# Performance work log

Measured on AMD Instinct MI355X. Metric: run time of the kernel, lower is better.

The kernel has to match this reference:

```python
import jax, jax.numpy as jnp
import numpy as np
from jax import lax

EMBED = 200
HID = 300
NCLASS = 2
B = 64
S = 255          # complete binary tree: 2**8 - 1 nodes
DEPTH = 8        # levels 0..7, root at node 0
VOCAB = 32000


def make_tree():
    parent = np.zeros(S, np.int32)
    parent[0] = S  # sentinel: root has no parent (dropped via dummy segment)
    for i in range(1, S):
        parent[i] = (i - 1) // 2
    depth = np.floor(np.log2(np.arange(S) + 1)).astype(np.int32)
    return jnp.asarray(parent), jnp.asarray(depth)


def setup_inputs() -> dict:
    key = jax.random.key(0)
    ks = jax.random.split(key, 8)
    parent, depth = make_tree()
    return {
        "x": jax.random.randint(ks[0], (S, B), 0, VOCAB, dtype=jnp.int32),
        "parent": parent,
        "depth": depth,
        "embed": jax.random.normal(ks[1], (VOCAB, EMBED), jnp.float32) * 0.1,
        "W_iou": jax.random.normal(ks[2], (EMBED, 3 * HID), jnp.float32) * 0.05,
        "U_iou": jax.random.normal(ks[3], (HID, 3 * HID), jnp.float32) * 0.05,
        "b_iou": jnp.zeros((3 * HID,), jnp.float32),
        "W_f": jax.random.normal(ks[4], (EMBED, HID), jnp.float32) * 0.05,
        "U_f": jax.random.normal(ks[5], (HID, HID), jnp.float32) * 0.05,
        "b_f": jnp.zeros((HID,), jnp.float32),
        "W_out": jax.random.normal(ks[6], (HID, NCLASS), jnp.float32) * 0.05,
        "b_out": jnp.zeros((NCLASS,), jnp.float32),
    }


def reference(x, parent, depth, embed, W_iou, U_iou, b_iou, W_f, U_f, b_f, W_out, b_out):
    # x: [S, B] token ids (seq-major, as in the torch model)
    emb = embed[x]                              # [S, B, E]
    wx_iou = emb @ W_iou + b_iou                # [S, B, 3H] input contributions
    wx_f = emb @ W_f + b_f                      # [S, B, H]
    seg = jnp.minimum(parent, S)                # root -> dummy segment S
    pidx = jnp.clip(parent, 0, S - 1)           # safe gather index for parent's x-part

    H0 = jnp.zeros((S, B, HID), emb.dtype)
    C0 = jnp.zeros((S, B, HID), emb.dtype)

    def level_step(carry, d):
        H, C = carry
        child = (depth == d + 1)[:, None, None].astype(H.dtype)   # nodes feeding level d
        # child-sum of hidden states into parents
        h_sum = jax.ops.segment_sum(H * child, seg, num_segments=S + 1)[:S]  # [S,B,H]
        # per-child forget gate: sigma(W_f x_parent + U_f h_child + b_f)
        f = jax.nn.sigmoid(wx_f[pidx] + H @ U_f)                  # [S,B,H]
        fc = jax.ops.segment_sum(f * C * child, seg, num_segments=S + 1)[:S]
        iou = wx_iou + h_sum @ U_iou                              # [S,B,3H]
        i_g, o_g, u_g = jnp.split(iou, 3, axis=-1)
        i_g = jax.nn.sigmoid(i_g)
        o_g = jax.nn.sigmoid(o_g)
        u_g = jnp.tanh(u_g)
        c_new = i_g * u_g + fc
        h_new = o_g * jnp.tanh(c_new)
        node = (depth == d)[:, None, None]
        H = jnp.where(node, h_new, H)
        C = jnp.where(node, c_new, C)
        return (H, C), None

    levels = jnp.arange(DEPTH - 1, -1, -1)      # process deepest level first
    (H, C), _ = lax.scan(level_step, (H0, C0), levels)

    tree_hidden = H[0]                          # [B, H] root hidden state
    logits = tree_hidden @ W_out + b_out        # Linear(hidden_dim, n_class)
    return jax.nn.log_softmax(logits, axis=-1)  # [B, 2]
```

## Files before the change

kernel.cpp:

```cpp
#include <hip/hip_runtime.h>
#include <hip/hip_bf16.h>
#include <math.h>

#define NS 255
#define NB 64
#define NE 200
#define NH 300
#define TS 2048
#define HTS 1024


typedef __attribute__((ext_vector_type(8))) short short8;
typedef __attribute__((ext_vector_type(4))) float f32x4;

__device__ __forceinline__ float sigmoidf_(float x) { return 1.0f / (1.0f + __expf(-x)); }
__device__ __forceinline__ unsigned short f2bf(float v) {
    union { __hip_bfloat16 b; unsigned short u; } cv; cv.b = __float2bfloat16(v); return cv.u;
}
__device__ __forceinline__ float bf2f(unsigned short u) {
    union { unsigned short u; __hip_bfloat16 b; } cv; cv.u = u; return __bfloat162float(cv.b);
}
__device__ __forceinline__ unsigned short f2h(float v) {
    union { _Float16 h; unsigned short u; } cv; cv.h = (_Float16)v; return cv.u;
}
__device__ __forceinline__ float h2f(unsigned short u) {
    union { unsigned short u; _Float16 h; } cv; cv.u = u; return (float)cv.h;
}
__device__ __forceinline__ int swz(int row, int kk) {
    int g = (kk >> 3) ^ ((row >> 1) & 3);
    return ((row << 2) + g) * 8 + (kk & 7);
}

__global__ __launch_bounds__(256) void prep_kernel(
    const float* __restrict__ U_iou, const float* __restrict__ U_f,
    const float* __restrict__ W_iou, const float* __restrict__ W_f,
    const float* __restrict__ embed, const int* __restrict__ x,
    unsigned short* __restrict__ BW, unsigned short* __restrict__ AembT)
{
    const int gBW = 4 * 5 * 17 * 256;
    const int gAe = NS * 7 * 256;
    int total = gBW + gAe;
    int stride = gridDim.x * blockDim.x;
    for (int gi = blockIdx.x * blockDim.x + threadIdx.x; gi < total; gi += stride) {
        unsigned short st[8];
        if (gi < gBW) {
            int gg = gi & 255, tile = gi >> 8;
            int row = gg >> 2, pos = gg & 3;
            int kk0 = (pos ^ ((row >> 1) & 3)) << 3;
            int c = tile % 17, t2 = tile / 17;
            int s = t2 % 5, g4 = t2 / 5;
            int j = s * 64 + row;
#pragma unroll
            for (int u = 0; u < 8; ++u) {
                int kk = kk0 + u; float v = 0.f;
                if (c < 7) {
                    int k = c * 32 + kk;
                    if (j < NH && k < NE)
                        v = (g4 < 3) ? W_iou[k * 900 + g4 * NH + j] : W_f[k * NH + j];
                } else {
                    int k = (c - 7) * 32 + kk;
                    if (j < NH && k < NH)
                        v = (g4 < 3) ? U_iou[k * 900 + g4 * NH + j] : U_f[k * NH + j];
                }
                st[u] = f2bf(v);
            }
            *(short8*)(BW + (size_t)tile * TS + (row * 4 + pos) * 8) = *(short8*)st;
        } else {
            int gi2 = gi - gBW;
            int gg = gi2 & 255, tile = gi2 >> 8;
            int row = gg >> 2, pos = gg & 3;
            int kk0 = (pos ^ ((row >> 1) & 3)) << 3;
            int c = tile % 7, node = tile / 7;
            int k0 = c * 32 + kk0;
            const float* er = embed + (size_t)x[node * NB + row] * NE;
#pragma unroll
            for (int u = 0; u < 8; ++u)
                st[u] = (k0 + u < NE) ? f2bf(er[k0 + u]) : (unsigned short)0;
            *(short8*)(AembT + (size_t)tile * TS + (row * 4 + pos) * 8) = *(short8*)st;
        }
    }
}

template<int NCH, int SA>
__device__ __forceinline__ void gemm2(f32x4 acc[4][2],
    const unsigned short* __restrict__ A, const unsigned short* __restrict__ B)
{
#pragma unroll
    for (int c = 0; c < NCH; ++c) {
        const unsigned short* At = A + c * SA;
        const unsigned short* Bt = B + c * TS;
        short8 a0 = *(const short8*)(At);
        short8 a1 = *(const short8*)(At + 512);
#pragma unroll
        for (int t = 0; t < 4; ++t) {
            short8 b = *(const short8*)(Bt + t * 512);
            acc[t][0] = __builtin_amdgcn_mfma_f32_16x16x32_bf16(a0, b, acc[t][0], 0, 0, 0);
            acc[t][1] = __builtin_amdgcn_mfma_f32_16x16x32_bf16(a1, b, acc[t][1], 0, 0, 0);
        }
    }
}
template<int NCH>
__device__ __forceinline__ void gemm_f(f32x4 acc[4][4],
    const unsigned short* __restrict__ A, const unsigned short* __restrict__ B)
{
#pragma unroll
    for (int c = 0; c < NCH; ++c) {
        const unsigned short* At = A + c * TS;
        const unsigned short* Bt = B + c * TS;
        short8 a0 = *(const short8*)(At);
        short8 a1 = *(const short8*)(At + 512);
        short8 a2 = *(const short8*)(At + 1024);
        short8 a3 = *(const short8*)(At + 1536);
#pragma unroll
        for (int t = 0; t < 4; ++t) {
            short8 b = *(const short8*)(Bt + t * 512);
            acc[t][0] = __builtin_amdgcn_mfma_f32_16x16x32_bf16(a0, b, acc[t][0], 0, 0, 0);
            acc[t][1] = __builtin_amdgcn_mfma_f32_16x16x32_bf16(a1, b, acc[t][1], 0, 0, 0);
            acc[t][2] = __builtin_amdgcn_mfma_f32_16x16x32_bf16(a2, b, acc[t][2], 0, 0, 0);
            acc[t][3] = __builtin_amdgcn_mfma_f32_16x16x32_bf16(a3, b, acc[t][3], 0, 0, 0);
        }
    }
}

__global__ __launch_bounds__(320) void level_kernel(
    const unsigned short* __restrict__ AembT, const unsigned short* __restrict__ BW,
    const float* __restrict__ b_iou, const float* __restrict__ b_f,
    unsigned short* __restrict__ HbfT, unsigned short* __restrict__ Cg,
    int base, int m, int sh)
{
    __shared__ unsigned short sm[24 * HTS];
    int bid = blockIdx.x;
    int p, s, half;
    if (m > 0) {
        int xcd = bid & 7, idx = bid >> 3;
        int o = idx % m, rest = idx / m;
        p = base + xcd * m + o;
        s = rest % 5; half = rest / 5;
    } else {
        int xcd = bid & 7;
        if (xcd & ((1 << sh) - 1)) return;
        p = base + (xcd >> sh);
        int idx = bid >> 3;
        s = idx % 5; half = idx / 5;
    }
    int tid = threadIdx.x;
    int w = tid >> 6, lane = tid & 63, ln = lane & 15, quad = lane >> 4;
    int l = 2 * p + 1, r = 2 * p + 2;
    int bsel = (w < 4) ? w : 3;
    int gq = (quad ^ ((ln >> 1) & 3)) * 8;
    int offA = (half * 32 + ln) * 32 + gq;
    int offL = ln * 32 + gq;
    int offB = ln * 32 + gq;

    for (int idx = w; idx < 24; idx += 5) {
        const unsigned short* gsrc;
        if (idx < 20) {
            int node = (idx < 10) ? l : r;
            int tt = (idx < 10) ? idx : idx - 10;
            gsrc = HbfT + ((size_t)node * 10 + tt) * TS + half * HTS;
        } else {
            int ii = idx - 20;
            int node = (ii < 2) ? l : r;
            gsrc = Cg + ((size_t)node * 10 + 2 * s + (ii & 1)) * TS + half * HTS;
        }
        unsigned short* ldst = sm + idx * HTS;
#pragma unroll
        for (int u = 0; u < 2; ++u)
            __builtin_amdgcn_global_load_lds(
                (const __attribute__((address_space(1))) unsigned short*)(gsrc + u * 512 + lane * 8),
                (__attribute__((address_space(3))) unsigned short*)(ldst + u * 512 + lane * 8),
                16, 0, 0);
    }

    f32x4 acc[4][2];
#pragma unroll
    for (int t = 0; t < 4; ++t)
#pragma unroll
        for (int q = 0; q < 2; ++q) acc[t][q] = (f32x4){0.f, 0.f, 0.f, 0.f};

    const unsigned short* Bsrc = BW + (size_t)(bsel * 5 + s) * 17 * TS;
    const unsigned short* Ae = AembT + (size_t)p * 7 * TS;
    gemm2<7, TS>(acc, Ae + offA, Bsrc + offB);

    __syncthreads();

    const unsigned short* BH = Bsrc + 7 * TS + offB;
    if (w < 3) {
        gemm2<10, HTS>(acc, sm + offL, BH);
        gemm2<10, HTS>(acc, sm + 10 * HTS + offL, BH);
    } else if (w == 3) {
        gemm2<10, HTS>(acc, sm + offL, BH);
    } else {
        gemm2<10, HTS>(acc, sm + 10 * HTS + offL, BH);
    }

    float* smf = (float*)sm;
    for (int t = 0; t < 4; ++t) {
        __syncthreads();
#pragma unroll
        for (int ms = 0; ms < 2; ++ms)
#pragma unroll
            for (int rr = 0; rr < 4; ++rr)
                smf[w * 544 + (ms * 16 + quad * 4 + rr) * 17 + ln] = acc[t][ms][rr];
        __syncthreads();
        for (int idx2 = tid; idx2 < 512; idx2 += 320) {
            int mm = idx2 >> 4, n = idx2 & 15;
            int gm = half * 32 + mm;
            int jj = s * 64 + t * 16 + n;
            bool ok = jj < NH;
            float pi = smf[0 * 544 + mm * 17 + n] + (ok ? b_iou[jj] : 0.f);
            float po = smf[1 * 544 + mm * 17 + n] + (ok ? b_iou[NH + jj] : 0.f);
            float pu = smf[2 * 544 + mm * 17 + n] + (ok ? b_iou[2 * NH + jj] : 0.f);
            float bj = ok ? b_f[jj] : 0.f;
            float fl = sigmoidf_(smf[3 * 544 + mm * 17 + n] + bj);
            float fr = sigmoidf_(smf[4 * 544 + mm * 17 + n] + bj);
            int xr = (mm >> 1) & 3;
            int cel = (mm * 4 + ((((t & 1) * 2) + (n >> 3)) ^ xr)) * 8 + (n & 7);
            int ts2 = t >> 1;
            float cl = h2f(sm[(20 + ts2) * HTS + cel]);
            float cr = h2f(sm[(22 + ts2) * HTS + cel]);
            float cc = sigmoidf_(pi) * tanhf(pu) + fl * cl + fr * cr;
            float hh = sigmoidf_(po) * tanhf(cc);
            size_t tbase = ((size_t)p * 10 + (jj >> 5)) * TS + swz(gm, jj & 31);
            if (ok) Cg[tbase] = f2h(cc);
            HbfT[tbase] = ok ? f2bf(hh) : (unsigned short)0;
        }
    }
}

__global__ __launch_bounds__(192) void leaf_kernel(
    const unsigned short* __restrict__ AembT, const unsigned short* __restrict__ BW,
    const float* __restrict__ b_iou,
    unsigned short* __restrict__ HbfT, unsigned short* __restrict__ Cg, int m)
{
    int bid = blockIdx.x;
    int xcd = bid & 7, idx = bid >> 3;
    int o = idx % m, rest = idx / m;
    int p = 127 + xcd * m + o;
    int s = rest % 5;
    int tid = threadIdx.x;
    int w = tid >> 6, lane = tid & 63, ln = lane & 15, quad = lane >> 4;
    int off = ln * 32 + (quad ^ ((ln >> 1) & 3)) * 8;

    const unsigned short* Bsrc = BW + (size_t)(w * 5 + s) * 17 * TS;
    const unsigned short* Ae = AembT + (size_t)p * 7 * TS;

    f32x4 acc[4][4];
#pragma unroll
    for (int t = 0; t < 4; ++t)
#pragma unroll
        for (int q = 0; q < 4; ++q) acc[t][q] = (f32x4){0.f, 0.f, 0.f, 0.f};

    gemm_f<7>(acc, Ae + off, Bsrc + off);

    __shared__ float tile[3][64][16];
    for (int t = 0; t < 4; ++t) {
        __syncthreads();
#pragma unroll
        for (int ms = 0; ms < 4; ++ms)
#pragma unroll
            for (int rr = 0; rr < 4; ++rr)
                tile[w][ms * 16 + quad * 4 + rr][ln] = acc[t][ms][rr];
        __syncthreads();
        for (int idx2 = tid; idx2 < 1024; idx2 += 192) {
            int mm = idx2 >> 4, n = idx2 & 15;
            int jj = s * 64 + t * 16 + n;
            bool ok = jj < NH;
            float pi = tile[0][mm][n] + (ok ? b_iou[jj] : 0.f);
            float po = tile[1][mm][n] + (ok ? b_iou[NH + jj] : 0.f);
            float pu = tile[2][mm][n] + (ok ? b_iou[2 * NH + jj] : 0.f);
            float cc = sigmoidf_(pi) * tanhf(pu);
            float hh = sigmoidf_(po) * tanhf(cc);
            size_t tbase = ((size_t)p * 10 + (jj >> 5)) * TS + swz(mm, jj & 31);
            if (ok) Cg[tbase] = f2h(cc);
            HbfT[tbase] = ok ? f2bf(hh) : (unsigned short)0;
        }
    }
}

__global__ __launch_bounds__(64) void out_kernel(
    const unsigned short* __restrict__ HbfT,
    const float* __restrict__ W_out, const float* __restrict__ b_out,
    float* __restrict__ out)
{
    int b = threadIdx.x;
    float l0 = 0.f, l1 = 0.f;
#pragma unroll 4
    for (int k = 0; k < NH; ++k) {
        float hk = bf2f(HbfT[(size_t)(k >> 5) * TS + swz(b, k & 31)]);
        l0 += hk * W_out[k * 2];
        l1 += hk * W_out[k * 2 + 1];
    }
    l0 += b_out[0];
    l1 += b_out[1];
    float m = fmaxf(l0, l1);
    float lse = m + logf(__expf(l0 - m) + __expf(l1 - m));
    out[b * 2 + 0] = l0 - lse;
    out[b * 2 + 1] = l1 - lse;
}

extern "C" void kernel_launch(void* const* d_in, const int* in_sizes, int n_in,
                              void* d_out, int out_size, void* d_ws, size_t ws_size,
                              hipStream_t stream)
{
    const int*   x     = (const int*)d_in[0];
    const float* embed = (const float*)d_in[3];
    const float* W_iou = (const float*)d_in[4];
    const float* U_iou = (const float*)d_in[5];
    const float* b_iou = (const float*)d_in[6];
    const float* W_f   = (const float*)d_in[7];
    const float* U_f   = (const float*)d_in[8];
    const float* b_f   = (const float*)d_in[9];
    const float* W_out = (const float*)d_in[10];
    const float* b_out = (const float*)d_in[11];

    char* ws = (char*)d_ws;
    unsigned short* HbfT  = (unsigned short*)(ws + 0);
    unsigned short* Cg    = (unsigned short*)(ws + 10444800);
    unsigned short* AembT = (unsigned short*)(ws + 20889600);
    unsigned short* BW    = (unsigned short*)(ws + 28200960);

    prep_kernel<<<4096, 256, 0, stream>>>(U_iou, U_f, W_iou, W_f, embed, x, BW, AembT);

    leaf_kernel<<<640, 192, 0, stream>>>(AembT, BW, b_iou, HbfT, Cg, 16);
    for (int d = 6; d >= 3; --d) {
        int base = (1 << d) - 1;
        int m = 1 << (d - 3);
        level_kernel<<<80 * m, 320, 0, stream>>>(AembT, BW, b_iou, b_f, HbfT, Cg,
                                                 base, m, 0);
    }
    for (int d = 2; d >= 0; --d) {
        level_kernel<<<80, 320, 0, stream>>>(AembT, BW, b_iou, b_f, HbfT, Cg,
                                             (1 << d) - 1, 0, 3 - d);
    }
    out_kernel<<<1, 64, 0, stream>>>(HbfT, W_out, b_out, (float*)d_out);
}
```

Before: 274.9 us.

## Fuse all tree-LSTM stages into one persistent kernel with grid barriers

Merges the prep, leaf, seven per-level and output kernels into a single persistent kernel of 512 blocks. Stages are separated by a custom two-phase atomic grid barrier in which eight leader blocks gather arrivals, so the inter-launch gaps are removed. In exchange the level work is mapped onto a fixed grid, leaf work now runs with 320 threads where only three waves compute, and correctness depends on all 512 blocks being co-resident and on the barrier's memory ordering.

```diff
diff --git a/kernel.cpp b/kernel.cpp
--- a/kernel.cpp
+++ b/kernel.cpp
@@ -8,6 +8,7 @@
 #define NH 300
 #define TS 2048
 #define HTS 1024
+#define NBLK 512
 
 
 typedef __attribute__((ext_vector_type(8))) short short8;
@@ -31,54 +32,20 @@
     return ((row << 2) + g) * 8 + (kk & 7);
 }
 
-__global__ __launch_bounds__(256) void prep_kernel(
-    const float* __restrict__ U_iou, const float* __restrict__ U_f,
-    const float* __restrict__ W_iou, const float* __restrict__ W_f,
-    const float* __restrict__ embed, const int* __restrict__ x,
-    unsigned short* __restrict__ BW, unsigned short* __restrict__ AembT)
-{
-    const int gBW = 4 * 5 * 17 * 256;
-    const int gAe = NS * 7 * 256;
-    int total = gBW + gAe;
-    int stride = gridDim.x * blockDim.x;
-    for (int gi = blockIdx.x * blockDim.x + threadIdx.x; gi < total; gi += stride) {
-        unsigned short st[8];
-        if (gi < gBW) {
-            int gg = gi & 255, tile = gi >> 8;
-            int row = gg >> 2, pos = gg & 3;
-            int kk0 = (pos ^ ((row >> 1) & 3)) << 3;
-            int c = tile % 17, t2 = tile / 17;
-            int s = t2 % 5, g4 = t2 / 5;
-            int j = s * 64 + row;
-#pragma unroll
-            for (int u = 0; u < 8; ++u) {
-                int kk = kk0 + u; float v = 0.f;
-                if (c < 7) {
-                    int k = c * 32 + kk;
-                    if (j < NH && k < NE)
-                        v = (g4 < 3) ? W_iou[k * 900 + g4 * NH + j] : W_f[k * NH + j];
-                } else {
-                    int k = (c - 7) * 32 + kk;
-                    if (j < NH && k < NH)
-                        v = (g4 < 3) ? U_iou[k * 900 + g4 * NH + j] : U_f[k * NH + j];
-                }
-                st[u] = f2bf(v);
-            }
-            *(short8*)(BW + (size_t)tile * TS + (row * 4 + pos) * 8) = *(short8*)st;
-        } else {
-            int gi2 = gi - gBW;
-            int gg = gi2 & 255, tile = gi2 >> 8;
-            int row = gg >> 2, pos = gg & 3;
-            int kk0 = (pos ^ ((row >> 1) & 3)) << 3;
-            int c = tile % 7, node = tile / 7;
-            int k0 = c * 32 + kk0;
-            const float* er = embed + (size_t)x[node * NB + row] * NE;
-#pragma unroll
-            for (int u = 0; u < 8; ++u)
-                st[u] = (k0 + u < NE) ? f2bf(er[k0 + u]) : (unsigned short)0;
-            *(short8*)(AembT + (size_t)tile * TS + (row * 4 + pos) * 8) = *(short8*)st;
-        }
-    }
+__device__ __forceinline__ void gbar(int* c1, int* c2, int tid, int bid) {
+    __syncthreads();
+    if (tid == 0) {
+        __hip_atomic_fetch_add(c1, 1, __ATOMIC_RELAXED, __HIP_MEMORY_SCOPE_AGENT);
+        if (bid < 8) {
+            while (__hip_atomic_load(c1, __ATOMIC_RELAXED, __HIP_MEMORY_SCOPE_AGENT) < NBLK)
+                __builtin_amdgcn_s_sleep(2);
+            __builtin_amdgcn_fence(__ATOMIC_RELEASE, "agent");
+            __hip_atomic_fetch_add(c2, 1, __ATOMIC_RELAXED, __HIP_MEMORY_SCOPE_AGENT);
+        }
+        while (__hip_atomic_load(c2, __ATOMIC_RELAXED, __HIP_MEMORY_SCOPE_AGENT) < 8)
+            __builtin_amdgcn_s_sleep(2);
+    }
+    __syncthreads();
 }
 
 template<int NCH, int SA>
@@ -122,28 +89,13 @@
     }
 }
 
-__global__ __launch_bounds__(320) void level_kernel(
+__device__ __forceinline__ void do_internal(unsigned short* sm,
+    int p, int s, int half, int tid,
     const unsigned short* __restrict__ AembT, const unsigned short* __restrict__ BW,
     const float* __restrict__ b_iou, const float* __restrict__ b_f,
-    unsigned short* __restrict__ HbfT, unsigned short* __restrict__ Cg,
-    int base, int m, int sh)
-{
-    __shared__ unsigned short sm[24 * HTS];
-    int bid = blockIdx.x;
-    int p, s, half;
-    if (m > 0) {
-        int xcd = bid & 7, idx = bid >> 3;
-        int o = idx % m, rest = idx / m;
-        p = base + xcd * m + o;
-        s = rest % 5; half = rest / 5;
-    } else {
-        int xcd = bid & 7;
-        if (xcd & ((1 << sh) - 1)) return;
-        p = base + (xcd >> sh);
-        int idx = bid >> 3;
-        s = idx % 5; half = idx / 5;
-    }
-    int tid = threadIdx.x;
+    unsigned short* __restrict__ HbfT, unsigned short* __restrict__ Cg)
+{
+    __syncthreads();
     int w = tid >> 6, lane = tid & 63, ln = lane & 15, quad = lane >> 4;
     int l = 2 * p + 1, r = 2 * p + 2;
     int bsel = (w < 4) ? w : 3;
@@ -228,47 +180,44 @@
     }
 }
 
-__global__ __launch_bounds__(192) void leaf_kernel(
-    const unsigned short* __restrict__ AembT, const unsigned short* __restrict__ BW,
-    const float* __restrict__ b_iou,
-    unsigned short* __restrict__ HbfT, unsigned short* __restrict__ Cg, int m)
-{
-    int bid = blockIdx.x;
-    int xcd = bid & 7, idx = bid >> 3;
-    int o = idx % m, rest = idx / m;
-    int p = 127 + xcd * m + o;
-    int s = rest % 5;
-    int tid = threadIdx.x;
+__device__ __forceinline__ void do_leaf(unsigned short* sm, int p, int s,
+    int tid, const unsigned short* __restrict__ AembT,
+    const unsigned short* __restrict__ BW, const float* __restrict__ b_iou,
+    unsigned short* __restrict__ HbfT, unsigned short* __restrict__ Cg)
+{
+    __syncthreads();
     int w = tid >> 6, lane = tid & 63, ln = lane & 15, quad = lane >> 4;
     int off = ln * 32 + (quad ^ ((ln >> 1) & 3)) * 8;
 
-    const unsigned short* Bsrc = BW + (size_t)(w * 5 + s) * 17 * TS;
-    const unsigned short* Ae = AembT + (size_t)p * 7 * TS;
-
     f32x4 acc[4][4];
 #pragma unroll
     for (int t = 0; t < 4; ++t)
 #pragma unroll
         for (int q = 0; q < 4; ++q) acc[t][q] = (f32x4){0.f, 0.f, 0.f, 0.f};
 
-    gemm_f<7>(acc, Ae + off, Bsrc + off);
-
-    __shared__ float tile[3][64][16];
+    if (w < 3) {
+        const unsigned short* Bsrc = BW + (size_t)(w * 5 + s) * 17 * TS;
+        const unsigned short* Ae = AembT + (size_t)p * 7 * TS;
+        gemm_f<7>(acc, Ae + off, Bsrc + off);
+    }
+
+    float* tile = (float*)sm;
     for (int t = 0; t < 4; ++t) {
         __syncthreads();
-#pragma unroll
-        for (int ms = 0; ms < 4; ++ms)
-#pragma unroll
-            for (int rr = 0; rr < 4; ++rr)
-                tile[w][ms * 16 + quad * 4 + rr][ln] = acc[t][ms][rr];
+        if (w < 3)
+#pragma unroll
+            for (int ms = 0; ms < 4; ++ms)
+#pragma unroll
+                for (int rr = 0; rr < 4; ++rr)
+                    tile[(w * 64 + ms * 16 + quad * 4 + rr) * 16 + ln] = acc[t][ms][rr];
         __syncthreads();
-        for (int idx2 = tid; idx2 < 1024; idx2 += 192) {
+        for (int idx2 = tid; idx2 < 1024; idx2 += 320) {
             int mm = idx2 >> 4, n = idx2 & 15;
             int jj = s * 64 + t * 16 + n;
             bool ok = jj < NH;
-            float pi = tile[0][mm][n] + (ok ? b_iou[jj] : 0.f);
-            float po = tile[1][mm][n] + (ok ? b_iou[NH + jj] : 0.f);
-            float pu = tile[2][mm][n] + (ok ? b_iou[2 * NH + jj] : 0.f);
+            float pi = tile[(0 * 64 + mm) * 16 + n] + (ok ? b_iou[jj] : 0.f);
+            float po = tile[(1 * 64 + mm) * 16 + n] + (ok ? b_iou[NH + jj] : 0.f);
+            float pu = tile[(2 * 64 + mm) * 16 + n] + (ok ? b_iou[2 * NH + jj] : 0.f);
             float cc = sigmoidf_(pi) * tanhf(pu);
             float hh = sigmoidf_(po) * tanhf(cc);
             size_t tbase = ((size_t)p * 10 + (jj >> 5)) * TS + swz(mm, jj & 31);
@@ -278,25 +227,108 @@
     }
 }
 
-__global__ __launch_bounds__(64) void out_kernel(
-    const unsigned short* __restrict__ HbfT,
+__global__ __launch_bounds__(320, 4) void fused_kernel(
+    const float* __restrict__ U_iou, const float* __restrict__ U_f,
+    const float* __restrict__ W_iou, const float* __restrict__ W_f,
+    const float* __restrict__ embed, const int* __restrict__ x,
+    const float* __restrict__ b_iou, const float* __restrict__ b_f,
     const float* __restrict__ W_out, const float* __restrict__ b_out,
-    float* __restrict__ out)
-{
-    int b = threadIdx.x;
-    float l0 = 0.f, l1 = 0.f;
+    unsigned short* __restrict__ BW, unsigned short* __restrict__ AembT,
+    unsigned short* __restrict__ HbfT, unsigned short* __restrict__ Cg,
+    float* __restrict__ out, int* __restrict__ bar)
+{
+    __shared__ unsigned short sm[24 * HTS];
+    int bid = blockIdx.x;
+    int tid = threadIdx.x;
+
+    {
+        const int gBW = 4 * 5 * 17 * 256;
+        const int gAe = NS * 7 * 256;
+        int total = gBW + gAe;
+        int stride = NBLK * 320;
+        for (int gi = bid * 320 + tid; gi < total; gi += stride) {
+            unsigned short st[8];
+            if (gi < gBW) {
+                int gg = gi & 255, tile = gi >> 8;
+                int row = gg >> 2, pos = gg & 3;
+                int kk0 = (pos ^ ((row >> 1) & 3)) << 3;
+                int c = tile % 17, t2 = tile / 17;
+                int s = t2 % 5, g4 = t2 / 5;
+                int j = s * 64 + row;
+#pragma unroll
+                for (int u = 0; u < 8; ++u) {
+                    int kk = kk0 + u; float v = 0.f;
+                    if (c < 7) {
+                        int k = c * 32 + kk;
+                        if (j < NH && k < NE)
+                            v = (g4 < 3) ? W_iou[k * 900 + g4 * NH + j] : W_f[k * NH + j];
+                    } else {
+                        int k = (c - 7) * 32 + kk;
+                        if (j < NH && k < NH)
+                            v = (g4 < 3) ? U_iou[k * 900 + g4 * NH + j] : U_f[k * NH + j];
+                    }
+                    st[u] = f2bf(v);
+                }
+                *(short8*)(BW + (size_t)tile * TS + (row * 4 + pos) * 8) = *(short8*)st;
+            } else {
+                int gi2 = gi - gBW;
+                int gg = gi2 & 255, tile = gi2 >> 8;
+                int row = gg >> 2, pos = gg & 3;
+                int kk0 = (pos ^ ((row >> 1) & 3)) << 3;
+                int c = tile % 7, node = tile / 7;
+                int k0 = c * 32 + kk0;
+                const float* er = embed + (size_t)x[node * NB + row] * NE;
+#pragma unroll
+                for (int u = 0; u < 8; ++u)
+                    st[u] = (k0 + u < NE) ? f2bf(er[k0 + u]) : (unsigned short)0;
+                *(short8*)(AembT + (size_t)tile * TS + (row * 4 + pos) * 8) = *(short8*)st;
+            }
+        }
+    }
+    gbar(bar + 0, bar + 1, tid, bid);
+
+    int xcd = bid & 7, slot = bid >> 3;
+
+    for (int t = slot; t < 80; t += 64)
+        do_leaf(sm, 127 + xcd * 16 + (t & 15), t >> 4, tid, AembT, BW, b_iou, HbfT, Cg);
+    gbar(bar + 2, bar + 3, tid, bid);
+
+    int bi = 4;
+    for (int d = 6; d >= 3; --d) {
+        int base = (1 << d) - 1;
+        int m = 1 << (d - 3);
+        int T = m * 10;
+        for (int t = slot; t < T; t += 64) {
+            int o = t % m, rest = t / m;
+            do_internal(sm, base + xcd * m + o, rest % 5, rest / 5,
+                        tid, AembT, BW, b_iou, b_f, HbfT, Cg);
+        }
+        gbar(bar + bi, bar + bi + 1, tid, bid); bi += 2;
+    }
+    for (int d = 2; d >= 0; --d) {
+        int n = 1 << d, sh = 3 - d;
+        if ((xcd & ((1 << sh) - 1)) == 0 && (xcd >> sh) < n && slot < 10)
+            do_internal(sm, n - 1 + (xcd >> sh), slot % 5, slot / 5,
+                        tid, AembT, BW, b_iou, b_f, HbfT, Cg);
+        gbar(bar + bi, bar + bi + 1, tid, bid); bi += 2;
+    }
+
+    if (bid == 0 && tid < NB) {
+        int b = tid;
+        float l0 = 0.f, l1 = 0.f;
 #pragma unroll 4
-    for (int k = 0; k < NH; ++k) {
-        float hk = bf2f(HbfT[(size_t)(k >> 5) * TS + swz(b, k & 31)]);
-        l0 += hk * W_out[k * 2];
-        l1 += hk * W_out[k * 2 + 1];
-    }
-    l0 += b_out[0];
-    l1 += b_out[1];
-    float m = fmaxf(l0, l1);
-    float lse = m + logf(__expf(l0 - m) + __expf(l1 - m));
-    out[b * 2 + 0] = l0 - lse;
-    out[b * 2 + 1] = l1 - lse;
+        for (int k = 0; k < NH; ++k) {
+            float hk = bf2f(HbfT[(size_t)(k >> 5) * TS + swz(b, k & 31)]);
+            l0 += hk * W_out[k * 2];
+            l1 += hk * W_out[k * 2 + 1];
+        }
+        l0 += b_out[0];
+        l1 += b_out[1];
+        float mx = fmaxf(l0, l1);
+        float lse = mx + logf(__expf(l0 - mx) + __expf(l1 - mx));
+        out[b * 2 + 0] = l0 - lse;
+        out[b * 2 + 1] = l1 - lse;
+    }
 }
 
 extern "C" void kernel_launch(void* const* d_in, const int* in_sizes, int n_in,
@@ -319,19 +351,11 @@
     unsigned short* Cg    = (unsigned short*)(ws + 10444800);
     unsigned short* AembT = (unsigned short*)(ws + 20889600);
     unsigned short* BW    = (unsigned short*)(ws + 28200960);
-
-    prep_kernel<<<4096, 256, 0, stream>>>(U_iou, U_f, W_iou, W_f, embed, x, BW, AembT);
-
-    leaf_kernel<<<640, 192, 0, stream>>>(AembT, BW, b_iou, HbfT, Cg, 16);
-    for (int d = 6; d >= 3; --d) {
-        int base = (1 << d) - 1;
-        int m = 1 << (d - 3);
-        level_kernel<<<80 * m, 320, 0, stream>>>(AembT, BW, b_iou, b_f, HbfT, Cg,
-                                                 base, m, 0);
-    }
-    for (int d = 2; d >= 0; --d) {
-        level_kernel<<<80, 320, 0, stream>>>(AembT, BW, b_iou, b_f, HbfT, Cg,
-                                             (1 << d) - 1, 0, 3 - d);
-    }
-    out_kernel<<<1, 64, 0, stream>>>(HbfT, W_out, b_out, (float*)d_out);
-}
+    int*            bar   = (int*)(ws + 29593600);
+
+    hipMemsetAsync(bar, 0, 128, stream);
+    fused_kernel<<<NBLK, 320, 0, stream>>>(U_iou, U_f, W_iou, W_f, embed, x,
+                                           b_iou, b_f, W_out, b_out,
+                                           BW, AembT, HbfT, Cg,
+                                           (float*)d_out, bar);
+}
```

After: 618.6 us. 2.25x slower.

## Fuse embedding gather into GEMMs and merge upper tree levels into persistent kernel

Applied to the files above, without the earlier changes.

Removes the precomputed bf16 embedding tile buffer: leaf and level kernels now gather embedding rows directly and convert to bf16 while loading MFMA operands. The five upper tree levels (depth 4 down to root) plus the output head are fused into one persistent 160-block kernel that uses global atomic counters as grid barriers, with agent-scope stores for H/C. This is meant to cut launch overhead and the prep pass that wrote the embedding tiles. In exchange it adds unswizzled scalar float gathers in the GEMM loop and relies on all 160 blocks being co-resident for the spin barriers.

```diff
diff --git a/kernel.cpp b/kernel.cpp
--- a/kernel.cpp
+++ b/kernel.cpp
@@ -30,67 +30,62 @@
     int g = (kk >> 3) ^ ((row >> 1) & 3);
     return ((row << 2) + g) * 8 + (kk & 7);
 }
+__device__ __forceinline__ void st_u16(unsigned short* p, unsigned short v) {
+    __hip_atomic_store(p, v, __ATOMIC_RELAXED, __HIP_MEMORY_SCOPE_AGENT);
+}
 
 __global__ __launch_bounds__(256) void prep_kernel(
     const float* __restrict__ U_iou, const float* __restrict__ U_f,
     const float* __restrict__ W_iou, const float* __restrict__ W_f,
-    const float* __restrict__ embed, const int* __restrict__ x,
-    unsigned short* __restrict__ BW, unsigned short* __restrict__ AembT)
-{
-    const int gBW = 4 * 5 * 17 * 256;
-    const int gAe = NS * 7 * 256;
-    int total = gBW + gAe;
-    int stride = gridDim.x * blockDim.x;
-    for (int gi = blockIdx.x * blockDim.x + threadIdx.x; gi < total; gi += stride) {
-        unsigned short st[8];
-        if (gi < gBW) {
-            int gg = gi & 255, tile = gi >> 8;
-            int row = gg >> 2, pos = gg & 3;
-            int kk0 = (pos ^ ((row >> 1) & 3)) << 3;
-            int c = tile % 17, t2 = tile / 17;
-            int s = t2 % 5, g4 = t2 / 5;
-            int j = s * 64 + row;
-#pragma unroll
-            for (int u = 0; u < 8; ++u) {
-                int kk = kk0 + u; float v = 0.f;
-                if (c < 7) {
-                    int k = c * 32 + kk;
-                    if (j < NH && k < NE)
-                        v = (g4 < 3) ? W_iou[k * 900 + g4 * NH + j] : W_f[k * NH + j];
-                } else {
-                    int k = (c - 7) * 32 + kk;
-                    if (j < NH && k < NH)
-                        v = (g4 < 3) ? U_iou[k * 900 + g4 * NH + j] : U_f[k * NH + j];
-                }
-                st[u] = f2bf(v);
-            }
-            *(short8*)(BW + (size_t)tile * TS + (row * 4 + pos) * 8) = *(short8*)st;
+    unsigned short* __restrict__ BW)
+{
+    int gi = blockIdx.x * blockDim.x + threadIdx.x;
+    if (gi >= 4 * 5 * 17 * 256) return;
+    unsigned short st[8];
+    int gg = gi & 255, tile = gi >> 8;
+    int row = gg >> 2, pos = gg & 3;
+    int kk0 = (pos ^ ((row >> 1) & 3)) << 3;
+    int c = tile % 17, t2 = tile / 17;
+    int s = t2 % 5, g4 = t2 / 5;
+    int j = s * 64 + row;
+#pragma unroll
+    for (int u = 0; u < 8; ++u) {
+        int kk = kk0 + u; float v = 0.f;
+        if (c < 7) {
+            int k = c * 32 + kk;
+            if (j < NH && k < NE)
+                v = (g4 < 3) ? W_iou[k * 900 + g4 * NH + j] : W_f[k * NH + j];
         } else {
-            int gi2 = gi - gBW;
-            int gg = gi2 & 255, tile = gi2 >> 8;
-            int row = gg >> 2, pos = gg & 3;
-            int kk0 = (pos ^ ((row >> 1) & 3)) << 3;
-            int c = tile % 7, node = tile / 7;
-            int k0 = c * 32 + kk0;
-            const float* er = embed + (size_t)x[node * NB + row] * NE;
-#pragma unroll
-            for (int u = 0; u < 8; ++u)
-                st[u] = (k0 + u < NE) ? f2bf(er[k0 + u]) : (unsigned short)0;
-            *(short8*)(AembT + (size_t)tile * TS + (row * 4 + pos) * 8) = *(short8*)st;
-        }
-    }
-}
-
-template<int NCH, int SA>
-__device__ __forceinline__ void gemm2(f32x4 acc[4][2],
-    const unsigned short* __restrict__ A, const unsigned short* __restrict__ B)
-{
-#pragma unroll
-    for (int c = 0; c < NCH; ++c) {
-        const unsigned short* At = A + c * SA;
+            int k = (c - 7) * 32 + kk;
+            if (j < NH && k < NH)
+                v = (g4 < 3) ? U_iou[k * 900 + g4 * NH + j] : U_f[k * NH + j];
+        }
+        st[u] = f2bf(v);
+    }
+    *(short8*)(BW + (size_t)tile * TS + (row * 4 + pos) * 8) = *(short8*)st;
+}
+
+__device__ __forceinline__ short8 ldcvt(const float* __restrict__ e, int k0) {
+    short8 r = (short8)(short)0;
+    if (k0 < NE) {
+        const float* p = e + k0;
+#pragma unroll
+        for (int u = 0; u < 8; ++u)
+            ((unsigned short*)&r)[u] = f2bf(p[u]);
+    }
+    return r;
+}
+
+__device__ __forceinline__ void gemm_emb2(f32x4 acc[4][2],
+    const float* __restrict__ e0, const float* __restrict__ e1,
+    const unsigned short* __restrict__ B, int quad)
+{
+#pragma unroll
+    for (int c = 0; c < 7; ++c) {
+        int k0 = c * 32 + quad * 8;
+        short8 a0 = ldcvt(e0, k0);
+        short8 a1 = ldcvt(e1, k0);
         const unsigned short* Bt = B + c * TS;
-        short8 a0 = *(const short8*)(At);
-        short8 a1 = *(const short8*)(At + 512);
 #pragma unroll
         for (int t = 0; t < 4; ++t) {
             short8 b = *(const short8*)(Bt + t * 512);
@@ -99,18 +94,19 @@
         }
     }
 }
-template<int NCH>
-__device__ __forceinline__ void gemm_f(f32x4 acc[4][4],
-    const unsigned short* __restrict__ A, const unsigned short* __restrict__ B)
-{
-#pragma unroll
-    for (int c = 0; c < NCH; ++c) {
-        const unsigned short* At = A + c * TS;
+__device__ __forceinline__ void gemm_emb4(f32x4 acc[4][4],
+    const float* __restrict__ e0, const float* __restrict__ e1,
+    const float* __restrict__ e2, const float* __restrict__ e3,
+    const unsigned short* __restrict__ B, int quad)
+{
+#pragma unroll
+    for (int c = 0; c < 7; ++c) {
+        int k0 = c * 32 + quad * 8;
+        short8 a0 = ldcvt(e0, k0);
+        short8 a1 = ldcvt(e1, k0);
+        short8 a2 = ldcvt(e2, k0);
+        short8 a3 = ldcvt(e3, k0);
         const unsigned short* Bt = B + c * TS;
-        short8 a0 = *(const short8*)(At);
-        short8 a1 = *(const short8*)(At + 512);
-        short8 a2 = *(const short8*)(At + 1024);
-        short8 a3 = *(const short8*)(At + 1536);
 #pragma unroll
         for (int t = 0; t < 4; ++t) {
             short8 b = *(const short8*)(Bt + t * 512);
@@ -121,34 +117,37 @@
         }
     }
 }
-
-__global__ __launch_bounds__(320) void level_kernel(
-    const unsigned short* __restrict__ AembT, const unsigned short* __restrict__ BW,
+template<int NCH>
+__device__ __forceinline__ void gemm_h(f32x4 acc[4][2],
+    const unsigned short* __restrict__ A, const unsigned short* __restrict__ B)
+{
+#pragma unroll
+    for (int c = 0; c < NCH; ++c) {
+        const unsigned short* At = A + c * HTS;
+        const unsigned short* Bt = B + c * TS;
+        short8 a0 = *(const short8*)(At);
+        short8 a1 = *(const short8*)(At + 512);
+#pragma unroll
+        for (int t = 0; t < 4; ++t) {
+            short8 b = *(const short8*)(Bt + t * 512);
+            acc[t][0] = __builtin_amdgcn_mfma_f32_16x16x32_bf16(a0, b, acc[t][0], 0, 0, 0);
+            acc[t][1] = __builtin_amdgcn_mfma_f32_16x16x32_bf16(a1, b, acc[t][1], 0, 0, 0);
+        }
+    }
+}
+
+__device__ __forceinline__ void internal_body(unsigned short* sm,
+    int p, int s, int half, int tid,
+    const int* __restrict__ x, const float* __restrict__ embed,
+    const unsigned short* __restrict__ BW,
     const float* __restrict__ b_iou, const float* __restrict__ b_f,
-    unsigned short* __restrict__ HbfT, unsigned short* __restrict__ Cg,
-    int base, int m, int sh)
-{
-    __shared__ unsigned short sm[24 * HTS];
-    int bid = blockIdx.x;
-    int p, s, half;
-    if (m > 0) {
-        int xcd = bid & 7, idx = bid >> 3;
-        int o = idx % m, rest = idx / m;
-        p = base + xcd * m + o;
-        s = rest % 5; half = rest / 5;
-    } else {
-        int xcd = bid & 7;
-        if (xcd & ((1 << sh) - 1)) return;
-        p = base + (xcd >> sh);
-        int idx = bid >> 3;
-        s = idx % 5; half = idx / 5;
-    }
-    int tid = threadIdx.x;
+    unsigned short* __restrict__ HbfT, unsigned short* __restrict__ Cg, int devst)
+{
+    __syncthreads();
     int w = tid >> 6, lane = tid & 63, ln = lane & 15, quad = lane >> 4;
     int l = 2 * p + 1, r = 2 * p + 2;
     int bsel = (w < 4) ? w : 3;
     int gq = (quad ^ ((ln >> 1) & 3)) * 8;
-    int offA = (half * 32 + ln) * 32 + gq;
     int offL = ln * 32 + gq;
     int offB = ln * 32 + gq;
 
@@ -179,19 +178,21 @@
         for (int q = 0; q < 2; ++q) acc[t][q] = (f32x4){0.f, 0.f, 0.f, 0.f};
 
     const unsigned short* Bsrc = BW + (size_t)(bsel * 5 + s) * 17 * TS;
-    const unsigned short* Ae = AembT + (size_t)p * 7 * TS;
-    gemm2<7, TS>(acc, Ae + offA, Bsrc + offB);
+    int row0 = half * 32 + ln;
+    const float* e0 = embed + (size_t)x[p * NB + row0] * NE;
+    const float* e1 = embed + (size_t)x[p * NB + row0 + 16] * NE;
+    gemm_emb2(acc, e0, e1, Bsrc + offB, quad);
 
     __syncthreads();
 
     const unsigned short* BH = Bsrc + 7 * TS + offB;
     if (w < 3) {
-        gemm2<10, HTS>(acc, sm + offL, BH);
-        gemm2<10, HTS>(acc, sm + 10 * HTS + offL, BH);
+        gemm_h<10>(acc, sm + offL, BH);
+        gemm_h<10>(acc, sm + 10 * HTS + offL, BH);
     } else if (w == 3) {
-        gemm2<10, HTS>(acc, sm + offL, BH);
+        gemm_h<10>(acc, sm + offL, BH);
     } else {
-        gemm2<10, HTS>(acc, sm + 10 * HTS + offL, BH);
+        gemm_h<10>(acc, sm + 10 * HTS + offL, BH);
     }
 
     float* smf = (float*)sm;
@@ -222,28 +223,53 @@
             float cc = sigmoidf_(pi) * tanhf(pu) + fl * cl + fr * cr;
             float hh = sigmoidf_(po) * tanhf(cc);
             size_t tbase = ((size_t)p * 10 + (jj >> 5)) * TS + swz(gm, jj & 31);
-            if (ok) Cg[tbase] = f2h(cc);
-            HbfT[tbase] = ok ? f2bf(hh) : (unsigned short)0;
-        }
-    }
-}
-
-__global__ __launch_bounds__(192) void leaf_kernel(
-    const unsigned short* __restrict__ AembT, const unsigned short* __restrict__ BW,
-    const float* __restrict__ b_iou,
-    unsigned short* __restrict__ HbfT, unsigned short* __restrict__ Cg, int m)
-{
+            unsigned short cv = f2h(cc);
+            unsigned short hv = ok ? f2bf(hh) : (unsigned short)0;
+            if (devst) {
+                if (ok) st_u16(&Cg[tbase], cv);
+                st_u16(&HbfT[tbase], hv);
+            } else {
+                if (ok) Cg[tbase] = cv;
+                HbfT[tbase] = hv;
+            }
+        }
+    }
+}
+
+__global__ __launch_bounds__(320) void level_kernel(
+    const int* __restrict__ x, const float* __restrict__ embed,
+    const unsigned short* __restrict__ BW,
+    const float* __restrict__ b_iou, const float* __restrict__ b_f,
+    unsigned short* __restrict__ HbfT, unsigned short* __restrict__ Cg,
+    int base, int m)
+{
+    __shared__ unsigned short sm[24 * HTS];
     int bid = blockIdx.x;
     int xcd = bid & 7, idx = bid >> 3;
     int o = idx % m, rest = idx / m;
-    int p = 127 + xcd * m + o;
-    int s = rest % 5;
+    int p = base + xcd * m + o;
+    internal_body(sm, p, rest % 5, rest / 5, threadIdx.x,
+                  x, embed, BW, b_iou, b_f, HbfT, Cg, 0);
+}
+
+__global__ __launch_bounds__(192) void leaf_kernel(
+    const int* __restrict__ x, const float* __restrict__ embed,
+    const unsigned short* __restrict__ BW, const float* __restrict__ b_iou,
+    unsigned short* __restrict__ HbfT, unsigned short* __restrict__ Cg)
+{
+    int bid = blockIdx.x;
+    int xcd = bid & 7, idx = bid >> 3;
+    int o = idx % 16, s = idx / 16;
+    int p = 127 + xcd * 16 + o;
     int tid = threadIdx.x;
     int w = tid >> 6, lane = tid & 63, ln = lane & 15, quad = lane >> 4;
-    int off = ln * 32 + (quad ^ ((ln >> 1) & 3)) * 8;
+    int offB = ln * 32 + (quad ^ ((ln >> 1) & 3)) * 8;
 
     const unsigned short* Bsrc = BW + (size_t)(w * 5 + s) * 17 * TS;
-    const unsigned short* Ae = AembT + (size_t)p * 7 * TS;
+    const float* e0 = embed + (size_t)x[p * NB + ln] * NE;
+    const float* e1 = embed + (size_t)x[p * NB + ln + 16] * NE;
+    const float* e2 = embed + (size_t)x[p * NB + ln + 32] * NE;
+    const float* e3 = embed + (size_t)x[p * NB + ln + 48] * NE;
 
     f32x4 acc[4][4];
 #pragma unroll
@@ -251,7 +277,7 @@
 #pragma unroll
         for (int q = 0; q < 4; ++q) acc[t][q] = (f32x4){0.f, 0.f, 0.f, 0.f};
 
-    gemm_f<7>(acc, Ae + off, Bsrc + off);
+    gemm_emb4(acc, e0, e1, e2, e3, Bsrc + offB, quad);
 
     __shared__ float tile[3][64][16];
     for (int t = 0; t < 4; ++t) {
@@ -278,25 +304,68 @@
     }
 }
 
-__global__ __launch_bounds__(64) void out_kernel(
-    const unsigned short* __restrict__ HbfT,
+__device__ __forceinline__ void tbar(int* c, int tid) {
+    __syncthreads();
+    if (tid == 0) {
+        __hip_atomic_fetch_add(c, 1, __ATOMIC_RELAXED, __HIP_MEMORY_SCOPE_AGENT);
+        while (__hip_atomic_load(c, __ATOMIC_RELAXED, __HIP_MEMORY_SCOPE_AGENT) < 160)
+            __builtin_amdgcn_s_sleep(2);
+    }
+    __syncthreads();
+}
+
+__global__ __launch_bounds__(320) void tail_kernel(
+    const int* __restrict__ x, const float* __restrict__ embed,
+    const unsigned short* __restrict__ BW,
+    const float* __restrict__ b_iou, const float* __restrict__ b_f,
     const float* __restrict__ W_out, const float* __restrict__ b_out,
-    float* __restrict__ out)
-{
-    int b = threadIdx.x;
-    float l0 = 0.f, l1 = 0.f;
+    unsigned short* __restrict__ HbfT, unsigned short* __restrict__ Cg,
+    float* __restrict__ out, int* __restrict__ bar)
+{
+    __shared__ unsigned short sm[24 * HTS];
+    int bid = blockIdx.x, tid = threadIdx.x;
+
+    {
+        int p = 15 + (bid & 15), rest = bid >> 4;
+        internal_body(sm, p, rest % 5, rest / 5, tid, x, embed, BW, b_iou, b_f, HbfT, Cg, 1);
+    }
+    tbar(bar + 0, tid);
+    if (bid < 80) {
+        int p = 7 + (bid & 7), rest = bid >> 3;
+        internal_body(sm, p, rest % 5, rest / 5, tid, x, embed, BW, b_iou, b_f, HbfT, Cg, 1);
+    }
+    tbar(bar + 1, tid);
+    if (bid < 40) {
+        int p = 3 + (bid & 3), rest = bid >> 2;
+        internal_body(sm, p, rest % 5, rest / 5, tid, x, embed, BW, b_iou, b_f, HbfT, Cg, 1);
+    }
+    tbar(bar + 2, tid);
+    if (bid < 20) {
+        int p = 1 + (bid & 1), rest = bid >> 1;
+        internal_body(sm, p, rest % 5, rest / 5, tid, x, embed, BW, b_iou, b_f, HbfT, Cg, 1);
+    }
+    tbar(bar + 3, tid);
+    if (bid < 10) {
+        internal_body(sm, 0, bid % 5, bid / 5, tid, x, embed, BW, b_iou, b_f, HbfT, Cg, 1);
+    }
+    tbar(bar + 4, tid);
+
+    if (bid == 0 && tid < NB) {
+        int b = tid;
+        float l0 = 0.f, l1 = 0.f;
 #pragma unroll 4
-    for (int k = 0; k < NH; ++k) {
-        float hk = bf2f(HbfT[(size_t)(k >> 5) * TS + swz(b, k & 31)]);
-        l0 += hk * W_out[k * 2];
-        l1 += hk * W_out[k * 2 + 1];
-    }
-    l0 += b_out[0];
-    l1 += b_out[1];
-    float m = fmaxf(l0, l1);
-    float lse = m + logf(__expf(l0 - m) + __expf(l1 - m));
-    out[b * 2 + 0] = l0 - lse;
-    out[b * 2 + 1] = l1 - lse;
+        for (int k = 0; k < NH; ++k) {
+            float hk = bf2f(HbfT[(size_t)(k >> 5) * TS + swz(b, k & 31)]);
+            l0 += hk * W_out[k * 2];
+            l1 += hk * W_out[k * 2 + 1];
+        }
+        l0 += b_out[0];
+        l1 += b_out[1];
+        float mx = fmaxf(l0, l1);
+        float lse = mx + logf(__expf(l0 - mx) + __expf(l1 - mx));
+        out[b * 2 + 0] = l0 - lse;
+        out[b * 2 + 1] = l1 - lse;
+    }
 }
 
 extern "C" void kernel_launch(void* const* d_in, const int* in_sizes, int n_in,
@@ -315,23 +384,16 @@
     const float* b_out = (const float*)d_in[11];
 
     char* ws = (char*)d_ws;
-    unsigned short* HbfT  = (unsigned short*)(ws + 0);
-    unsigned short* Cg    = (unsigned short*)(ws + 10444800);
-    unsigned short* AembT = (unsigned short*)(ws + 20889600);
-    unsigned short* BW    = (unsigned short*)(ws + 28200960);
-
-    prep_kernel<<<4096, 256, 0, stream>>>(U_iou, U_f, W_iou, W_f, embed, x, BW, AembT);
-
-    leaf_kernel<<<640, 192, 0, stream>>>(AembT, BW, b_iou, HbfT, Cg, 16);
-    for (int d = 6; d >= 3; --d) {
-        int base = (1 << d) - 1;
-        int m = 1 << (d - 3);
-        level_kernel<<<80 * m, 320, 0, stream>>>(AembT, BW, b_iou, b_f, HbfT, Cg,
-                                                 base, m, 0);
-    }
-    for (int d = 2; d >= 0; --d) {
-        level_kernel<<<80, 320, 0, stream>>>(AembT, BW, b_iou, b_f, HbfT, Cg,
-                                             (1 << d) - 1, 0, 3 - d);
-    }
-    out_kernel<<<1, 64, 0, stream>>>(HbfT, W_out, b_out, (float*)d_out);
-}
+    unsigned short* HbfT = (unsigned short*)(ws + 0);
+    unsigned short* Cg   = (unsigned short*)(ws + 10444800);
+    unsigned short* BW   = (unsigned short*)(ws + 28200960);
+    int*            bar  = (int*)(ws + 29593600);
+
+    hipMemsetAsync(bar, 0, 64, stream);
+    prep_kernel<<<340, 256, 0, stream>>>(U_iou, U_f, W_iou, W_f, BW);
+    leaf_kernel<<<640, 192, 0, stream>>>(x, embed, BW, b_iou, HbfT, Cg);
+    level_kernel<<<640, 320, 0, stream>>>(x, embed, BW, b_iou, b_f, HbfT, Cg, 63, 8);
+    level_kernel<<<320, 320, 0, stream>>>(x, embed, BW, b_iou, b_f, HbfT, Cg, 31, 4);
+    tail_kernel<<<160, 320, 0, stream>>>(x, embed, BW, b_iou, b_f, W_out, b_out,
+                                         HbfT, Cg, (float*)d_out, bar);
+}
```

New measurement: 304.6 us. +10.8%, slower.
